# Kernel tuning notes

Hardware: AMD Instinct MI355X
Metric: run time of the kernel (lower is better)

Reference implementation:

```python
import jax, jax.numpy as jnp
import numpy as np

SEQ, BATCH, IN, HID = 2048, 64, 256, 256


def setup_inputs() -> dict:
    key = jax.random.key(0)
    ks = jax.random.split(key, 9)
    s_in = 1.0 / np.sqrt(IN)
    s_h = 1.0 / np.sqrt(HID)
    return {
        "x": jax.random.normal(ks[0], (SEQ, BATCH, IN), dtype=jnp.float32),
        "hidden": jnp.zeros((BATCH, HID), dtype=jnp.float32),
        # torch nn.Linear params: weight (out, in), bias (out,)
        "Wz": jax.random.uniform(ks[1], (HID, IN), jnp.float32, -s_in, s_in),
        "bz": jax.random.uniform(ks[2], (HID,), jnp.float32, -s_in, s_in),
        "Uz": jax.random.uniform(ks[3], (HID, HID), jnp.float32, -s_h, s_h),
        "cz": jax.random.uniform(ks[4], (HID,), jnp.float32, -s_h, s_h),
        "Wh": jax.random.uniform(ks[5], (HID, IN), jnp.float32, -s_in, s_in),
        "bh": jax.random.uniform(ks[6], (HID,), jnp.float32, -s_in, s_in),
        "Uh": jax.random.uniform(ks[7], (HID, HID), jnp.float32, -s_h, s_h),
        "ch": jax.random.uniform(ks[8], (HID,), jnp.float32, -s_h, s_h),
    }


def reference(x, hidden, Wz, bz, Uz, cz, Wh, bh, Uh, ch):
    # Precompute all input projections in two batched GEMMs: (S,B,I)@(I,H)
    xz = jnp.einsum("sbi,hi->sbh", x, Wz) + bz  # W_z x_t + b_z
    xh = jnp.einsum("sbi,hi->sbh", x, Wh) + bh  # W_h x_t + b_h

    def step(h, inp):
        xz_t, xh_t = inp
        z = jax.nn.sigmoid(xz_t + h @ Uz.T + cz)
        h_tilde = jnp.tanh(xh_t + h @ Uh.T + ch)
        h_new = (1.0 - z) * h + z * h_tilde
        return h_new, h_new

    h_final, outputs = jax.lax.scan(step, hidden, (xz, xh))
    return outputs, h_final
```

## Files before the change

kernel.cpp:

```cpp
#include <hip/hip_runtime.h>
#include <math.h>

#define SEQ   2048
#define BATCH 64
#define IN    256
#define HID   256
#define NBLK  (SEQ / 8)

typedef _Float16 hf2 __attribute__((ext_vector_type(2)));
typedef _Float16 hf4 __attribute__((ext_vector_type(4)));
typedef _Float16 hf8 __attribute__((ext_vector_type(8)));
typedef float    f32x2 __attribute__((ext_vector_type(2)));
typedef float    f32x4 __attribute__((ext_vector_type(4)));

static __device__ __forceinline__ float fast_sigmoid(float x) {
    return __builtin_amdgcn_rcpf(1.0f + __expf(-x));
}

static __device__ __forceinline__ float fast_tanh(float x) {
    const float e = __expf(-2.0f * x);
    return fmaf(2.0f, __builtin_amdgcn_rcpf(1.0f + e), -1.0f);
}

static __device__ __forceinline__ hf8 cvt8(const float4& a, const float4& b) {
    hf8 f;
    f[0] = (_Float16)a.x; f[1] = (_Float16)a.y;
    f[2] = (_Float16)a.z; f[3] = (_Float16)a.w;
    f[4] = (_Float16)b.x; f[5] = (_Float16)b.y;
    f[6] = (_Float16)b.z; f[7] = (_Float16)b.w;
    return f;
}

static __device__ __forceinline__ void bar_lds() {
    asm volatile("s_waitcnt lgkmcnt(0)" ::: "memory");
    __builtin_amdgcn_s_barrier();
}

__global__ __launch_bounds__(256) void w16_kernel(
    const float* __restrict__ Wz, const float* __restrict__ Wh,
    _Float16* __restrict__ W16)
{
    const int idx = blockIdx.x * 256 + threadIdx.x;
    const int row = idx >> 8;
    const int col = idx & 255;
    const float v = (row < 256) ? Wz[row * 256 + col] : Wh[(row - 256) * 256 + col];
    W16[idx] = (_Float16)v;
}

__global__ __launch_bounds__(256) void proj_mfma_kernel(
    const float* __restrict__ x,
    const _Float16* __restrict__ W16,
    const float* __restrict__ bz, const float* __restrict__ cz,
    const float* __restrict__ bh, const float* __restrict__ ch,
    _Float16* __restrict__ xz16,
    float* __restrict__ xh_out)
{
    const int tid  = threadIdx.x;
    const int lane = tid & 63;
    const int w    = tid >> 6;
    const int m0   = blockIdx.x * 16;
    const int col0 = w * 128;

    const int r = lane & 15;
    const int g = lane >> 4;

    f32x4 acc[8] = {f32x4{0,0,0,0}, f32x4{0,0,0,0}, f32x4{0,0,0,0}, f32x4{0,0,0,0},
                    f32x4{0,0,0,0}, f32x4{0,0,0,0}, f32x4{0,0,0,0}, f32x4{0,0,0,0}};

    const float*    xrow  = x   + (size_t)(m0 + r) * IN + g * 8;
    const _Float16* wbase = W16 + (size_t)(col0 + r) * IN + g * 8;

#pragma unroll
    for (int kt = 0; kt < 8; ++kt) {
        const float4 xa = *reinterpret_cast<const float4*>(xrow + kt * 32);
        const float4 xb = *reinterpret_cast<const float4*>(xrow + kt * 32 + 4);
        const hf8 a = cvt8(xa, xb);
#pragma unroll
        for (int t = 0; t < 8; ++t) {
            const hf8 bfrag = *reinterpret_cast<const hf8*>(
                wbase + (size_t)t * 16 * IN + kt * 32);
            acc[t] = __builtin_amdgcn_mfma_f32_16x16x32_f16(a, bfrag, acc[t], 0, 0, 0);
        }
    }

    if (w < 2) {
#pragma unroll
        for (int t = 0; t < 8; ++t) {
            const int c = col0 + t * 16 + r;
            const float bsum = bz[c] + cz[c];
#pragma unroll
            for (int reg = 0; reg < 4; ++reg) {
                const int m = m0 + 4 * g + reg;
                xz16[(size_t)m * HID + c] = (_Float16)(acc[t][reg] + bsum);
            }
        }
    } else {
#pragma unroll
        for (int t = 0; t < 8; ++t) {
            const int c = col0 - 256 + t * 16 + r;
            const float bsum = bh[c] + ch[c];
#pragma unroll
            for (int reg = 0; reg < 4; ++reg) {
                const int m = m0 + 4 * g + reg;
                xh_out[(size_t)m * HID + c] = acc[t][reg] + bsum;
            }
        }
    }
}

__global__ __launch_bounds__(1024, 1) void rec_mfma_kernel(
    const float* __restrict__ hidden0,
    const float* __restrict__ Uz,
    const float* __restrict__ Uh,
    const _Float16* __restrict__ xz16,
    float* __restrict__ out,
    float* __restrict__ h_final)
{
    const int b    = blockIdx.x;
    const int tid  = threadIdx.x;
    const int w    = tid >> 6;
    const int lane = tid & 63;
    const int r    = lane & 15;
    const int g    = lane >> 4;

    __shared__ __align__(16) _Float16 hbuf[2][256];
    __shared__ __align__(16) float    sbuf[512];
    __shared__ __align__(16) _Float16 xzs[2][8][256];
    __shared__ __align__(16) float    xhs[2][8][256];

    hf8 au[2][8];
    {
        const float* usrc = (r & 1) ? Uh : Uz;
        const int    hrow = r >> 1;
#pragma unroll
        for (int i = 0; i < 2; ++i) {
            const int m = 2 * w + i;
            const float* p0 = usrc + (size_t)(8 * m + hrow) * HID;
#pragma unroll
            for (int kt = 0; kt < 8; ++kt) {
                const float* p = p0 + kt * 32 + 8 * g;
                au[i][kt] = cvt8(*reinterpret_cast<const float4*>(p),
                                 *reinterpret_cast<const float4*>(p + 4));
            }
        }
    }

    if (tid < 256) {
        hbuf[0][tid] = (_Float16)hidden0[b * HID + tid];
    }

    const int o = 16 * w + (lane & 15);
    float hp = 0.0f;
    float* pst = out + (size_t)b * HID + o;
    if (lane < 16) {
        hp = hidden0[b * HID + o];
    }

    const int srow = tid >> 7;
    const int scol = (tid & 127) * 2;
    hf2   rz;
    f32x2 rh;
    {
        const size_t a0 = ((size_t)srow * BATCH + b) * HID + scol;
        *reinterpret_cast<hf2*>(&xzs[0][srow][scol]) =
            *reinterpret_cast<const hf2*>(xz16 + a0);
        *reinterpret_cast<f32x2*>(&xhs[0][srow][scol]) =
            *reinterpret_cast<const f32x2*>(out + a0);
        const size_t a1 = ((size_t)(8 + srow) * BATCH + b) * HID + scol;
        rz = *reinterpret_cast<const hf2*>(xz16 + a1);
        rh = *reinterpret_cast<const f32x2*>(out + a1);
    }
    __syncthreads();

    for (int j = 0; j < NBLK; ++j) {
        const int jb = j & 1;
#pragma unroll
        for (int s = 0; s < 8; ++s) {
            float xzc = 0.0f, xhc = 0.0f;
            if (lane < 16) {
                xzc = (float)xzs[jb][s][o];
                xhc = xhs[jb][s][o];
            }
            f32x4 acc0{0, 0, 0, 0}, acc1{0, 0, 0, 0};
#pragma unroll
            for (int kt = 0; kt < 8; ++kt) {
                const hf8 bb = *reinterpret_cast<const hf8*>(
                    &hbuf[s & 1][kt * 32 + 8 * g]);
                acc0 = __builtin_amdgcn_mfma_f32_16x16x32_f16(
                    au[0][kt], bb, acc0, 0, 0, 0);
                acc1 = __builtin_amdgcn_mfma_f32_16x16x32_f16(
                    au[1][kt], bb, acc1, 0, 0, 0);
            }
            if (r == 0) {
                *reinterpret_cast<f32x4*>(&sbuf[(2 * w) * 16 + 4 * g])     = acc0;
                *reinterpret_cast<f32x4*>(&sbuf[(2 * w + 1) * 16 + 4 * g]) = acc1;
            }
            if (lane < 16) {
                const f32x2 pr = *reinterpret_cast<const f32x2*>(&sbuf[2 * o]);
                const float z  = fast_sigmoid(pr[0] + xzc);
                const float th = fast_tanh(pr[1] + xhc);
                hp = fmaf(z, th - hp, hp);
                *pst = hp;
                pst += (size_t)BATCH * HID;
                hbuf[(s + 1) & 1][o] = (_Float16)hp;
            }
            if (s == 7 && j + 1 < NBLK) {
                *reinterpret_cast<hf2*>(&xzs[jb ^ 1][srow][scol])   = rz;
                *reinterpret_cast<f32x2*>(&xhs[jb ^ 1][srow][scol]) = rh;
                int trow = 8 * (j + 2) + srow;
                if (trow >= SEQ) trow = SEQ - 1;
                const size_t an = ((size_t)trow * BATCH + b) * HID + scol;
                rz = *reinterpret_cast<const hf2*>(xz16 + an);
                rh = *reinterpret_cast<const f32x2*>(out + an);
            }
            bar_lds();
        }
    }

    if (lane < 16) {
        h_final[(size_t)b * HID + o] = hp;
    }
}

extern "C" void kernel_launch(void* const* d_in, const int* in_sizes, int n_in,
                              void* d_out, int out_size, void* d_ws, size_t ws_size,
                              hipStream_t stream) {
    const float* x      = (const float*)d_in[0];
    const float* hidden = (const float*)d_in[1];
    const float* Wz     = (const float*)d_in[2];
    const float* bz     = (const float*)d_in[3];
    const float* Uz     = (const float*)d_in[4];
    const float* cz     = (const float*)d_in[5];
    const float* Wh     = (const float*)d_in[6];
    const float* bh     = (const float*)d_in[7];
    const float* Uh     = (const float*)d_in[8];
    const float* ch     = (const float*)d_in[9];

    float* out     = (float*)d_out;
    float* h_final = out + (size_t)SEQ * BATCH * HID;

    _Float16* xz16 = (_Float16*)d_ws;
    _Float16* W16  = (_Float16*)((char*)d_ws + ((size_t)64 << 20));

    w16_kernel<<<512, 256, 0, stream>>>(Wz, Wh, W16);

    proj_mfma_kernel<<<(SEQ * BATCH) / 16, 256, 0, stream>>>(
        x, W16, bz, cz, bh, ch, xz16, out);

    rec_mfma_kernel<<<BATCH, 1024, 0, stream>>>(
        hidden, Uz, Uh, xz16, out, h_final);
}
```

Baseline: 2.081 ms.

## Replace MFMA recurrent matvec with per-thread fdot2 dot products and shuffle reduction

The recurrent step kernel no longer uses MFMA tiles with an LDS scratch exchange. Each of 1024 threads now owns one output row and a quarter of K, holding Uz/Uh rows in registers as half2 values. It computes the partial dot products with packed fdot2 and reduces across 4 lanes with xor shuffles. This removes the sbuf LDS round trip and the MFMA latency chain on the serial critical path, in exchange for more VALU work and broadcast LDS reads of h per thread.

```diff
diff --git a/kernel.cpp b/kernel.cpp
--- a/kernel.cpp
+++ b/kernel.cpp
@@ -12,6 +12,14 @@
 typedef _Float16 hf8 __attribute__((ext_vector_type(8)));
 typedef float    f32x2 __attribute__((ext_vector_type(2)));
 typedef float    f32x4 __attribute__((ext_vector_type(4)));
+
+static __device__ __forceinline__ float dot2(hf2 a, hf2 b, float c) {
+#if __has_builtin(__builtin_amdgcn_fdot2)
+    return __builtin_amdgcn_fdot2(a, b, c, false);
+#else
+    return fmaf((float)a.x, (float)b.x, fmaf((float)a.y, (float)b.y, c));
+#endif
+}
 
 static __device__ __forceinline__ float fast_sigmoid(float x) {
     return __builtin_amdgcn_rcpf(1.0f + __expf(-x));
@@ -108,7 +116,7 @@
     }
 }
 
-__global__ __launch_bounds__(1024, 1) void rec_mfma_kernel(
+__global__ __launch_bounds__(1024, 1) void rec_dot2_kernel(
     const float* __restrict__ hidden0,
     const float* __restrict__ Uz,
     const float* __restrict__ Uh,
@@ -116,45 +124,36 @@
     float* __restrict__ out,
     float* __restrict__ h_final)
 {
-    const int b    = blockIdx.x;
-    const int tid  = threadIdx.x;
-    const int w    = tid >> 6;
-    const int lane = tid & 63;
-    const int r    = lane & 15;
-    const int g    = lane >> 4;
+    const int b   = blockIdx.x;
+    const int tid = threadIdx.x;
+    const int og  = tid >> 2;
+    const int q   = tid & 3;
 
     __shared__ __align__(16) _Float16 hbuf[2][256];
-    __shared__ __align__(16) float    sbuf[512];
     __shared__ __align__(16) _Float16 xzs[2][8][256];
     __shared__ __align__(16) float    xhs[2][8][256];
 
-    hf8 au[2][8];
+    hf2 uz[32], uh[32];
     {
-        const float* usrc = (r & 1) ? Uh : Uz;
-        const int    hrow = r >> 1;
-#pragma unroll
-        for (int i = 0; i < 2; ++i) {
-            const int m = 2 * w + i;
-            const float* p0 = usrc + (size_t)(8 * m + hrow) * HID;
-#pragma unroll
-            for (int kt = 0; kt < 8; ++kt) {
-                const float* p = p0 + kt * 32 + 8 * g;
-                au[i][kt] = cvt8(*reinterpret_cast<const float4*>(p),
-                                 *reinterpret_cast<const float4*>(p + 4));
-            }
+        const float* pz = Uz + (size_t)og * HID + q * 64;
+        const float* ph = Uh + (size_t)og * HID + q * 64;
+#pragma unroll
+        for (int i = 0; i < 16; ++i) {
+            float4 v;
+            v = *reinterpret_cast<const float4*>(pz + 4 * i);
+            uz[2*i]   = hf2{(_Float16)v.x, (_Float16)v.y};
+            uz[2*i+1] = hf2{(_Float16)v.z, (_Float16)v.w};
+            v = *reinterpret_cast<const float4*>(ph + 4 * i);
+            uh[2*i]   = hf2{(_Float16)v.x, (_Float16)v.y};
+            uh[2*i+1] = hf2{(_Float16)v.z, (_Float16)v.w};
         }
     }
 
     if (tid < 256) {
         hbuf[0][tid] = (_Float16)hidden0[b * HID + tid];
     }
-
-    const int o = 16 * w + (lane & 15);
-    float hp = 0.0f;
-    float* pst = out + (size_t)b * HID + o;
-    if (lane < 16) {
-        hp = hidden0[b * HID + o];
-    }
+    float hp = hidden0[b * HID + og];
+    float* pst = out + (size_t)b * HID + og;
 
     const int srow = tid >> 7;
     const int scol = (tid & 127) * 2;
@@ -176,34 +175,51 @@
         const int jb = j & 1;
 #pragma unroll
         for (int s = 0; s < 8; ++s) {
-            float xzc = 0.0f, xhc = 0.0f;
-            if (lane < 16) {
-                xzc = (float)xzs[jb][s][o];
-                xhc = xhs[jb][s][o];
-            }
-            f32x4 acc0{0, 0, 0, 0}, acc1{0, 0, 0, 0};
-#pragma unroll
-            for (int kt = 0; kt < 8; ++kt) {
-                const hf8 bb = *reinterpret_cast<const hf8*>(
-                    &hbuf[s & 1][kt * 32 + 8 * g]);
-                acc0 = __builtin_amdgcn_mfma_f32_16x16x32_f16(
-                    au[0][kt], bb, acc0, 0, 0, 0);
-                acc1 = __builtin_amdgcn_mfma_f32_16x16x32_f16(
-                    au[1][kt], bb, acc1, 0, 0, 0);
-            }
-            if (r == 0) {
-                *reinterpret_cast<f32x4*>(&sbuf[(2 * w) * 16 + 4 * g])     = acc0;
-                *reinterpret_cast<f32x4*>(&sbuf[(2 * w + 1) * 16 + 4 * g]) = acc1;
-            }
-            if (lane < 16) {
-                const f32x2 pr = *reinterpret_cast<const f32x2*>(&sbuf[2 * o]);
-                const float z  = fast_sigmoid(pr[0] + xzc);
-                const float th = fast_tanh(pr[1] + xhc);
-                hp = fmaf(z, th - hp, hp);
+            const float xzc = (float)xzs[jb][s][og];
+            const float xhc = xhs[jb][s][og];
+            const _Float16* hsl = &hbuf[s & 1][q * 64];
+            float za = 0.f, zb = 0.f, ha = 0.f, hb = 0.f;
+#pragma unroll
+            for (int c8 = 0; c8 < 8; ++c8) {
+                const hf8 hv = *reinterpret_cast<const hf8*>(hsl + 8 * c8);
+                const hf2 p0 = __builtin_shufflevector(hv, hv, 0, 1);
+                const hf2 p1 = __builtin_shufflevector(hv, hv, 2, 3);
+                const hf2 p2 = __builtin_shufflevector(hv, hv, 4, 5);
+                const hf2 p3 = __builtin_shufflevector(hv, hv, 6, 7);
+                if (c8 & 1) {
+                    zb = dot2(p0, uz[4*c8+0], zb);
+                    zb = dot2(p1, uz[4*c8+1], zb);
+                    zb = dot2(p2, uz[4*c8+2], zb);
+                    zb = dot2(p3, uz[4*c8+3], zb);
+                    hb = dot2(p0, uh[4*c8+0], hb);
+                    hb = dot2(p1, uh[4*c8+1], hb);
+                    hb = dot2(p2, uh[4*c8+2], hb);
+                    hb = dot2(p3, uh[4*c8+3], hb);
+                } else {
+                    za = dot2(p0, uz[4*c8+0], za);
+                    za = dot2(p1, uz[4*c8+1], za);
+                    za = dot2(p2, uz[4*c8+2], za);
+                    za = dot2(p3, uz[4*c8+3], za);
+                    ha = dot2(p0, uh[4*c8+0], ha);
+                    ha = dot2(p1, uh[4*c8+1], ha);
+                    ha = dot2(p2, uh[4*c8+2], ha);
+                    ha = dot2(p3, uh[4*c8+3], ha);
+                }
+            }
+            float accz = za + zb;
+            float acch = ha + hb;
+            accz += __shfl_xor(accz, 1);
+            accz += __shfl_xor(accz, 2);
+            acch += __shfl_xor(acch, 1);
+            acch += __shfl_xor(acch, 2);
+            const float z  = fast_sigmoid(accz + xzc);
+            const float th = fast_tanh(acch + xhc);
+            hp = fmaf(z, th - hp, hp);
+            if (q == 0) {
                 *pst = hp;
-                pst += (size_t)BATCH * HID;
-                hbuf[(s + 1) & 1][o] = (_Float16)hp;
-            }
+                hbuf[(s + 1) & 1][og] = (_Float16)hp;
+            }
+            pst += (size_t)BATCH * HID;
             if (s == 7 && j + 1 < NBLK) {
                 *reinterpret_cast<hf2*>(&xzs[jb ^ 1][srow][scol])   = rz;
                 *reinterpret_cast<f32x2*>(&xhs[jb ^ 1][srow][scol]) = rh;
@@ -217,8 +233,8 @@
         }
     }
 
-    if (lane < 16) {
-        h_final[(size_t)b * HID + o] = hp;
+    if (q == 0) {
+        h_final[(size_t)b * HID + og] = hp;
     }
 }
 
@@ -247,6 +263,6 @@
     proj_mfma_kernel<<<(SEQ * BATCH) / 16, 256, 0, stream>>>(
         x, W16, bz, cz, bh, ch, xz16, out);
 
-    rec_mfma_kernel<<<BATCH, 1024, 0, stream>>>(
+    rec_dot2_kernel<<<BATCH, 1024, 0, stream>>>(
         hidden, Uz, Uh, xz16, out, h_final);
 }
```

Result: slower. 2.270 ms (+9.1%).

## Split recurrent matvec between MFMA waves and packed-dot VALU waves

Applied to the files above, without the earlier changes.

The recurrent kernel now gives outputs 0-127 to eight waves using MFMA and outputs 128-255 to the other eight waves, which compute dot products with fdot2 on the VALU. In the VALU waves, four lanes split each output and combine their partial sums with DPP adds. A padded, skewed copy of h is kept for the VALU reads to limit bank conflicts. The intent is to shorten the serial per-step matvec latency by running matrix and vector units at once, at the cost of extra LDS writes and extra code per step.

```diff
diff --git a/kernel.cpp b/kernel.cpp
--- a/kernel.cpp
+++ b/kernel.cpp
@@ -12,6 +12,21 @@
 typedef _Float16 hf8 __attribute__((ext_vector_type(8)));
 typedef float    f32x2 __attribute__((ext_vector_type(2)));
 typedef float    f32x4 __attribute__((ext_vector_type(4)));
+
+static __device__ __forceinline__ float dot2(hf2 a, hf2 b, float c) {
+#if __has_builtin(__builtin_amdgcn_fdot2)
+    return __builtin_amdgcn_fdot2(a, b, c, false);
+#else
+    return fmaf((float)a.x, (float)b.x, fmaf((float)a.y, (float)b.y, c));
+#endif
+}
+
+template <int CTRL>
+static __device__ __forceinline__ float dpp_add(float v) {
+    const int pv = __builtin_amdgcn_update_dpp(
+        0, __builtin_bit_cast(int, v), CTRL, 0xF, 0xF, true);
+    return v + __builtin_bit_cast(float, pv);
+}
 
 static __device__ __forceinline__ float fast_sigmoid(float x) {
     return __builtin_amdgcn_rcpf(1.0f + __expf(-x));
@@ -108,7 +123,7 @@
     }
 }
 
-__global__ __launch_bounds__(1024, 1) void rec_mfma_kernel(
+__global__ __launch_bounds__(1024, 1) void rec_hybrid_kernel(
     const float* __restrict__ hidden0,
     const float* __restrict__ Uz,
     const float* __restrict__ Uh,
@@ -120,16 +135,21 @@
     const int tid  = threadIdx.x;
     const int w    = tid >> 6;
     const int lane = tid & 63;
-    const int r    = lane & 15;
-    const int g    = lane >> 4;
-
-    __shared__ __align__(16) _Float16 hbuf[2][256];
-    __shared__ __align__(16) float    sbuf[512];
+    const bool m_wave = (w < 8);
+
+    const int r = lane & 15;
+    const int g = lane >> 4;
+    const int q   = lane & 3;
+    const int vog = 128 + (w - 8) * 16 + (lane >> 2);
+
+    __shared__ __align__(16) _Float16 hlin[2][256];
+    __shared__ __align__(16) _Float16 hsk[2][320];
+    __shared__ __align__(16) float    sbuf[256];
     __shared__ __align__(16) _Float16 xzs[2][8][256];
     __shared__ __align__(16) float    xhs[2][8][256];
 
-    hf8 au[2][8];
-    {
+    hf8 ureg[16];
+    if (m_wave) {
         const float* usrc = (r & 1) ? Uh : Uz;
         const int    hrow = r >> 1;
 #pragma unroll
@@ -139,22 +159,33 @@
 #pragma unroll
             for (int kt = 0; kt < 8; ++kt) {
                 const float* p = p0 + kt * 32 + 8 * g;
-                au[i][kt] = cvt8(*reinterpret_cast<const float4*>(p),
-                                 *reinterpret_cast<const float4*>(p + 4));
-            }
+                ureg[8 * i + kt] = cvt8(*reinterpret_cast<const float4*>(p),
+                                        *reinterpret_cast<const float4*>(p + 4));
+            }
+        }
+    } else {
+        const float* pz = Uz + (size_t)vog * HID + q * 64;
+        const float* ph = Uh + (size_t)vog * HID + q * 64;
+#pragma unroll
+        for (int c8 = 0; c8 < 8; ++c8) {
+            ureg[c8]     = cvt8(*reinterpret_cast<const float4*>(pz + 8 * c8),
+                                *reinterpret_cast<const float4*>(pz + 8 * c8 + 4));
+            ureg[8 + c8] = cvt8(*reinterpret_cast<const float4*>(ph + 8 * c8),
+                                *reinterpret_cast<const float4*>(ph + 8 * c8 + 4));
         }
     }
 
     if (tid < 256) {
-        hbuf[0][tid] = (_Float16)hidden0[b * HID + tid];
-    }
-
-    const int o = 16 * w + (lane & 15);
-    float hp = 0.0f;
-    float* pst = out + (size_t)b * HID + o;
-    if (lane < 16) {
-        hp = hidden0[b * HID + o];
-    }
+        const _Float16 h0 = (_Float16)hidden0[b * HID + tid];
+        hlin[0][tid] = h0;
+        hsk[0][tid + (tid >> 5) * 8] = h0;
+    }
+
+    const int mo = 16 * w + (lane & 15);
+    const int own_o = m_wave ? mo : vog;
+    float hp = hidden0[b * HID + (own_o & 255)];
+    float* pst = out + (size_t)b * HID + own_o;
+    const int osk = own_o + (own_o >> 5) * 8;
 
     const int srow = tid >> 7;
     const int scol = (tid & 127) * 2;
@@ -172,38 +203,89 @@
     }
     __syncthreads();
 
+#define UE(ri, e) __builtin_shufflevector(ureg[ri], ureg[ri], 2*(e), 2*(e)+1)
+
     for (int j = 0; j < NBLK; ++j) {
         const int jb = j & 1;
 #pragma unroll
         for (int s = 0; s < 8; ++s) {
-            float xzc = 0.0f, xhc = 0.0f;
-            if (lane < 16) {
-                xzc = (float)xzs[jb][s][o];
-                xhc = xhs[jb][s][o];
-            }
-            f32x4 acc0{0, 0, 0, 0}, acc1{0, 0, 0, 0};
-#pragma unroll
-            for (int kt = 0; kt < 8; ++kt) {
-                const hf8 bb = *reinterpret_cast<const hf8*>(
-                    &hbuf[s & 1][kt * 32 + 8 * g]);
-                acc0 = __builtin_amdgcn_mfma_f32_16x16x32_f16(
-                    au[0][kt], bb, acc0, 0, 0, 0);
-                acc1 = __builtin_amdgcn_mfma_f32_16x16x32_f16(
-                    au[1][kt], bb, acc1, 0, 0, 0);
-            }
-            if (r == 0) {
-                *reinterpret_cast<f32x4*>(&sbuf[(2 * w) * 16 + 4 * g])     = acc0;
-                *reinterpret_cast<f32x4*>(&sbuf[(2 * w + 1) * 16 + 4 * g]) = acc1;
-            }
-            if (lane < 16) {
-                const f32x2 pr = *reinterpret_cast<const f32x2*>(&sbuf[2 * o]);
-                const float z  = fast_sigmoid(pr[0] + xzc);
-                const float th = fast_tanh(pr[1] + xhc);
+            if (m_wave) {
+                const float xzc = (float)xzs[jb][s][mo];
+                const float xhc = xhs[jb][s][mo];
+                f32x4 acc0{0, 0, 0, 0}, acc1{0, 0, 0, 0};
+#pragma unroll
+                for (int kt = 0; kt < 8; ++kt) {
+                    const hf8 bb = *reinterpret_cast<const hf8*>(
+                        &hlin[s & 1][kt * 32 + 8 * g]);
+                    acc0 = __builtin_amdgcn_mfma_f32_16x16x32_f16(
+                        ureg[kt], bb, acc0, 0, 0, 0);
+                    acc1 = __builtin_amdgcn_mfma_f32_16x16x32_f16(
+                        ureg[8 + kt], bb, acc1, 0, 0, 0);
+                }
+                if (r == 0) {
+                    *reinterpret_cast<f32x4*>(&sbuf[(2 * w) * 16 + 4 * g])     = acc0;
+                    *reinterpret_cast<f32x4*>(&sbuf[(2 * w + 1) * 16 + 4 * g]) = acc1;
+                }
+                if (lane < 16) {
+                    const f32x2 pr = *reinterpret_cast<const f32x2*>(&sbuf[2 * mo]);
+                    const float z  = fast_sigmoid(pr[0] + xzc);
+                    const float th = fast_tanh(pr[1] + xhc);
+                    hp = fmaf(z, th - hp, hp);
+                    *pst = hp;
+                    const _Float16 hh = (_Float16)hp;
+                    hlin[(s + 1) & 1][mo] = hh;
+                    hsk[(s + 1) & 1][osk] = hh;
+                }
+            } else {
+                const float xzc = (float)xzs[jb][s][vog];
+                const float xhc = xhs[jb][s][vog];
+                const _Float16* hsl = &hsk[s & 1][q * 80];
+                float za = 0.f, zb = 0.f, ha = 0.f, hb = 0.f;
+#pragma unroll
+                for (int c8 = 0; c8 < 8; ++c8) {
+                    const int off = 8 * c8 + ((c8 >> 2) << 3);
+                    const hf8 hv = *reinterpret_cast<const hf8*>(hsl + off);
+                    const hf2 p0 = __builtin_shufflevector(hv, hv, 0, 1);
+                    const hf2 p1 = __builtin_shufflevector(hv, hv, 2, 3);
+                    const hf2 p2 = __builtin_shufflevector(hv, hv, 4, 5);
+                    const hf2 p3 = __builtin_shufflevector(hv, hv, 6, 7);
+                    if (c8 & 1) {
+                        zb = dot2(p0, UE(c8, 0), zb);
+                        zb = dot2(p1, UE(c8, 1), zb);
+                        zb = dot2(p2, UE(c8, 2), zb);
+                        zb = dot2(p3, UE(c8, 3), zb);
+                        hb = dot2(p0, UE(8 + c8, 0), hb);
+                        hb = dot2(p1, UE(8 + c8, 1), hb);
+                        hb = dot2(p2, UE(8 + c8, 2), hb);
+                        hb = dot2(p3, UE(8 + c8, 3), hb);
+                    } else {
+                        za = dot2(p0, UE(c8, 0), za);
+                        za = dot2(p1, UE(c8, 1), za);
+                        za = dot2(p2, UE(c8, 2), za);
+                        za = dot2(p3, UE(c8, 3), za);
+                        ha = dot2(p0, UE(8 + c8, 0), ha);
+                        ha = dot2(p1, UE(8 + c8, 1), ha);
+                        ha = dot2(p2, UE(8 + c8, 2), ha);
+                        ha = dot2(p3, UE(8 + c8, 3), ha);
+                    }
+                }
+                float accz = za + zb;
+                float acch = ha + hb;
+                accz = dpp_add<0xB1>(accz);
+                acch = dpp_add<0xB1>(acch);
+                accz = dpp_add<0x4E>(accz);
+                acch = dpp_add<0x4E>(acch);
+                const float z  = fast_sigmoid(accz + xzc);
+                const float th = fast_tanh(acch + xhc);
                 hp = fmaf(z, th - hp, hp);
-                *pst = hp;
-                pst += (size_t)BATCH * HID;
-                hbuf[(s + 1) & 1][o] = (_Float16)hp;
-            }
+                if (q == 0) {
+                    *pst = hp;
+                    const _Float16 hh = (_Float16)hp;
+                    hlin[(s + 1) & 1][vog] = hh;
+                    hsk[(s + 1) & 1][osk]  = hh;
+                }
+            }
+            pst += (size_t)BATCH * HID;
             if (s == 7 && j + 1 < NBLK) {
                 *reinterpret_cast<hf2*>(&xzs[jb ^ 1][srow][scol])   = rz;
                 *reinterpret_cast<f32x2*>(&xhs[jb ^ 1][srow][scol]) = rh;
@@ -216,9 +298,10 @@
             bar_lds();
         }
     }
-
-    if (lane < 16) {
-        h_final[(size_t)b * HID + o] = hp;
+#undef UE
+
+    if ((m_wave && lane < 16) || (!m_wave && q == 0)) {
+        h_final[(size_t)b * HID + own_o] = hp;
     }
 }
 
@@ -247,6 +330,6 @@
     proj_mfma_kernel<<<(SEQ * BATCH) / 16, 256, 0, stream>>>(
         x, W16, bz, cz, bh, ch, xz16, out);
 
-    rec_mfma_kernel<<<BATCH, 1024, 0, stream>>>(
+    rec_hybrid_kernel<<<BATCH, 1024, 0, stream>>>(
         hidden, Uz, Uh, xz16, out, h_final);
 }
```

New measurement: 2.039 ms. 1.02x faster.
